# Kernel tuning notes

Hardware: AMD Instinct MI355X
Metric: run time of the kernel (lower is better)

The kernel has to match this reference:

```python
import jax, jax.numpy as jnp
import numpy as np

B, A, C = 16, 16384, 81
TOP_K = 50
CONF_THRESH = 0.5
IOU_THRESH = 0.5
VAR0, VAR1 = 0.1, 0.2          # cfg['variance']
IMG_HW = 1.0                   # cfg['min_dim']/img_size = 320/320
MIN_SIZE = 0.0
NEG = -jnp.inf


def setup_inputs() -> dict:
    key = jax.random.key(0)
    k1, k2, k3 = jax.random.split(key, 3)
    conf_preds = jax.random.uniform(k1, (B, A, C), dtype=jnp.float32)
    loc_delta = jax.random.normal(k2, (B, A, 4), dtype=jnp.float32)
    anchors = jax.random.uniform(k3, (A, 4), dtype=jnp.float32)  # cxcywh priors in [0,1)
    return {"conf_preds": conf_preds, "loc_delta": loc_delta, "anchors": anchors}


def _decode_clip(loc, anchors):
    # SSD decode: cxcy = prior_cxcy + loc_xy*v0*prior_wh ; wh = prior_wh*exp(loc_wh*v1)
    cxcy = anchors[..., :2] + loc[..., :2] * VAR0 * anchors[..., 2:]
    wh = anchors[..., 2:] * jnp.exp(loc[..., 2:] * VAR1)
    x1y1 = cxcy - wh * 0.5
    x2y2 = x1y1 + wh
    boxes = jnp.concatenate([x1y1, x2y2], axis=-1)  # [..., 4] xyxy
    return jnp.clip(boxes, 0.0, IMG_HW)            # clip_boxes_to_image((1,1))


def _nms_single(boxes, s):
    # boxes: [A,4] xyxy, s: [A] scores with invalid entries already at -inf.
    # Greedy NMS, fixed TOP_K iterations (torchvision semantics: suppress iou > thresh).
    areas = (boxes[:, 2] - boxes[:, 0]) * (boxes[:, 3] - boxes[:, 1])

    def step(s, _):
        i = jnp.argmax(s)
        take = s[i] > NEG
        b = boxes[i]
        xx1 = jnp.maximum(b[0], boxes[:, 0])
        yy1 = jnp.maximum(b[1], boxes[:, 1])
        xx2 = jnp.minimum(b[2], boxes[:, 2])
        yy2 = jnp.minimum(b[3], boxes[:, 3])
        inter = jnp.maximum(xx2 - xx1, 0.0) * jnp.maximum(yy2 - yy1, 0.0)
        iou = inter / (areas[i] + areas - inter)
        s = jnp.where(take & (iou > IOU_THRESH), NEG, s)
        s = s.at[i].set(NEG)  # guarantee progress
        return s, (i, take)

    _, (idx, take) = jax.lax.scan(step, s, None, length=TOP_K)
    return idx, take  # [TOP_K] int, [TOP_K] bool


def reference(conf_preds, loc_delta, anchors):
    boxes = _decode_clip(loc_delta, anchors)                # [B,A,4]
    conf = jnp.transpose(conf_preds, (0, 2, 1))             # [B,C,A]
    # remove_small_boxes(min_size=0) as a mask (all-true here, kept for fidelity)
    w = boxes[..., 2] - boxes[..., 0]
    h = boxes[..., 3] - boxes[..., 1]
    valid = (w >= MIN_SIZE) & (h >= MIN_SIZE)               # [B,A]
    masked = jnp.where((conf > CONF_THRESH) & valid[:, None, :], conf, NEG)  # [B,C,A]

    sg = jax.lax.stop_gradient
    nms_c = jax.vmap(_nms_single, in_axes=(None, 0))        # over classes
    nms_bc = jax.vmap(nms_c, in_axes=(0, 0))                # over batch
    idx, take = nms_bc(sg(boxes), sg(masked))               # [B,C,K]

    scores_sel = jnp.take_along_axis(conf, idx, axis=2)     # [B,C,K]
    b_idx = jnp.arange(boxes.shape[0])[:, None, None]
    boxes_sel = boxes[b_idx, idx]                           # [B,C,K,4]
    preds = jnp.concatenate([
        jnp.where(take, scores_sel, 0.0)[..., None],
        jnp.where(take[..., None], boxes_sel, 0.0),
    ], axis=-1)                                             # [B,C,K,5]
    return preds
```

## Files before the change

### kernel.cpp

```cpp
#include <hip/hip_runtime.h>
#include <math.h>

#define NB 16
#define NA 16384
#define NC 81
#define TOPK 50
#define NBK 255
#define TRC 1024
#define NEGF (-__builtin_inff())
#define SUPC 0.5000000298023223876953125

typedef unsigned long long ull;

#define WS_CONFT_OFF  ((size_t)4194304)
#define WS_FULL  (WS_CONFT_OFF + (size_t)NB * NC * NA)

__device__ __forceinline__ bool iou_gt_half(float inter, float den) {
    return fmaf(den, -0.5f, inter) > den * 0x1p-25f;
}

__device__ __forceinline__ unsigned enc8(float v) {
    unsigned e = 0xFFu;
    if (v > 0.5f) {
        unsigned d = 255u - ((__float_as_uint(v) >> 15) & 0xFFu);
        e = (d > 254u) ? 254u : d;
    }
    return e;
}

__device__ __forceinline__ void decode_body(int i, const float* __restrict__ loc,
                                            const float* __restrict__ anc,
                                            float* __restrict__ boxes) {
#pragma clang fp contract(off)
    int a = i & (NA - 1);
    float4 an = ((const float4*)anc)[a];
    float4 ld = ((const float4*)loc)[i];
    float cx = an.x + (ld.x * 0.1f) * an.z;
    float cy = an.y + (ld.y * 0.1f) * an.w;
    float w = an.z * (float)exp((double)(ld.z * 0.2f));
    float h = an.w * (float)exp((double)(ld.w * 0.2f));
    float x1 = cx - w * 0.5f;
    float y1 = cy - h * 0.5f;
    float x2 = x1 + w;
    float y2 = y1 + h;
    x1 = fminf(fmaxf(x1, 0.f), 1.f);
    y1 = fminf(fmaxf(y1, 0.f), 1.f);
    x2 = fminf(fmaxf(x2, 0.f), 1.f);
    y2 = fminf(fmaxf(y2, 0.f), 1.f);
    ((float4*)boxes)[i] = make_float4(x1, y1, x2, y2);
}

__global__ __launch_bounds__(256) void decode_k(const float* __restrict__ loc,
                                                const float* __restrict__ anc,
                                                float* __restrict__ boxes) {
    int i = blockIdx.x * 256 + threadIdx.x;
    if (i < NB * NA) decode_body(i, loc, anc, boxes);
}

#define TSLAB 256
__global__ __launch_bounds__(256) void prep_k(const float* __restrict__ conf,
                                              const float* __restrict__ loc,
                                              const float* __restrict__ anc,
                                              float* __restrict__ boxes,
                                              unsigned char* __restrict__ confT) {
    __shared__ unsigned char code[TSLAB * NC];
    const int t = threadIdx.x;
    const int b = blockIdx.y, slab = blockIdx.x;
    decode_body(b * NA + slab * TSLAB + t, loc, anc, boxes);
    const float4* src = (const float4*)(conf + ((size_t)b * NA + (size_t)slab * TSLAB) * NC);
    for (int i = t; i < (TSLAB * NC) / 4; i += 256) {
        float4 v = src[i];
        unsigned wrd = enc8(v.x) | (enc8(v.y) << 8) | (enc8(v.z) << 16) | (enc8(v.w) << 24);
        *(unsigned*)&code[4 * i] = wrd;
    }
    __syncthreads();
    const int lane = t & 63, wv = t >> 6;
    for (int c = wv; c < NC; c += 4) {
        unsigned v = 0u;
#pragma unroll
        for (int j = 0; j < 4; ++j)
            v |= (unsigned)code[(4 * lane + j) * NC + c] << (8 * j);
        *(unsigned*)(confT + ((size_t)b * NC + c) * NA + (size_t)slab * TSLAB + 4 * lane) = v;
    }
}

#define HIST16(Q)                                                          \
    do {                                                                   \
        unsigned wrds_[4] = {(Q).x, (Q).y, (Q).z, (Q).w};                  \
        _Pragma("unroll")                                                  \
        for (int m_ = 0; m_ < 4; ++m_) {                                   \
            _Pragma("unroll")                                              \
            for (int k_ = 0; k_ < 4; ++k_) {                               \
                unsigned bk_ = (wrds_[m_] >> (8 * k_)) & 0xFFu;            \
                if (bk_ != 0xFFu) atomicAdd(&s_hist[wv][bk_], 1u);         \
            }                                                              \
        }                                                                  \
    } while (0)

#define SCAT16(Q, BA)                                                      \
    do {                                                                   \
        unsigned wrds_[4] = {(Q).x, (Q).y, (Q).z, (Q).w};                  \
        _Pragma("unroll")                                                  \
        for (int m_ = 0; m_ < 4; ++m_) {                                   \
            _Pragma("unroll")                                              \
            for (int k_ = 0; k_ < 4; ++k_) {                               \
                int bk_ = (int)((wrds_[m_] >> (8 * k_)) & 0xFFu);          \
                if (bk_ >= trLo && bk_ < trHi)                             \
                    s_ix[atomicAdd(&s_cur[bk_], 1u)] =                     \
                        (unsigned short)((BA) + 4 * m_ + k_);              \
            }                                                              \
        }                                                                  \
    } while (0)

__global__ __launch_bounds__(256, 8) void nmsB12_k(const unsigned char* __restrict__ confT,
                                                   const float* __restrict__ conf,
                                                   const float* __restrict__ boxes,
                                                   float* __restrict__ out) {
#pragma clang fp contract(off)
    const int blk = blockIdx.x;
    const int b = blk / NC, c = blk - b * NC;
    const int t = threadIdx.x;
    const int lane = t & 63, wv = t >> 6;

    __shared__ unsigned short s_ix[TRC];
    __shared__ unsigned s_off[NBK + 1];
    __shared__ unsigned s_hist[4][NBK + 2];
    __shared__ unsigned s_cur[NBK];
    __shared__ unsigned s_wsum[4];
    __shared__ float4 s_abox[TOPK];
    __shared__ float s_aarea[TOPK];
    __shared__ float4 s_cbox[256];
    __shared__ unsigned long long s_kill[4];
    __shared__ int s_ctrl[16];

    const uint4* row16 = (const uint4*)(confT + ((size_t)b * NC + c) * NA);
    const float* cp = conf + ((size_t)b * NA) * NC + c;
    const float4* bb = (const float4*)boxes + (size_t)b * NA;
    float* orow = out + ((size_t)b * NC + c) * (TOPK * 5);

    for (int i = t; i < 4 * (NBK + 2); i += 256) ((unsigned*)s_hist)[i] = 0u;
    if (t == 0) { s_ctrl[0] = 0; s_ctrl[8] = 0; s_ctrl[12] = 0; }
    __syncthreads();

#pragma unroll
    for (int r = 0; r < 4; ++r) {
        uint4 q = row16[t + 256 * r];
        HIST16(q);
    }
    __syncthreads();

    unsigned cnt = 0u;
    if (t < NBK) {
        cnt = s_hist[0][t] + s_hist[1][t] + s_hist[2][t] + s_hist[3][t];
        atomicMax(&s_ctrl[8], (int)cnt);
    }
    unsigned v = cnt;
#pragma unroll
    for (int off = 1; off < 64; off <<= 1) {
        unsigned o = __shfl_up(v, off);
        if (lane >= off) v += o;
    }
    if (lane == 63) s_wsum[wv] = v;
    __syncthreads();
    unsigned basep = 0u;
    for (int w2 = 0; w2 < wv; ++w2) basep += s_wsum[w2];
    v += basep;
    if (t < NBK) s_off[t + 1] = v;
    if (t == 0) s_off[0] = 0u;
    __syncthreads();

    if (s_ctrl[8] <= TRC) {
        while (true) {
            if (t == 0) {
                int lo = s_ctrl[12];
                int hi = lo;
                while (hi < NBK && s_off[hi + 1] - s_off[lo] <= (unsigned)TRC) hi++;
                s_ctrl[13] = hi;
            }
            __syncthreads();
            const int trLo = s_ctrl[12], trHi = s_ctrl[13];
            const unsigned tbase = s_off[trLo], tend = s_off[trHi];
            if (tbase == tend) break;
            for (int i = trLo + t; i < trHi; i += 256) s_cur[i] = s_off[i] - tbase;
            __syncthreads();
#pragma unroll
            for (int r = 0; r < 4; ++r) {
                uint4 q = row16[t + 256 * r];
                SCAT16(q, 16 * (t + 256 * r));
            }
            if (t == 0) s_ctrl[7] = trLo;
            __syncthreads();

            while (true) {
                if (t == 0) {
                    int bp = s_ctrl[7];
                    int mode;
                    if (bp >= trHi || s_off[bp] >= tend) {
                        mode = 2;
                    } else {
                        unsigned pos = s_off[bp] - tbase;
                        int bpl = bp;
                        unsigned q = pos;
                        for (int w = 0; w < 4; ++w) {
                            s_ctrl[2 + w] = (int)q;
                            while (bpl < trHi && (s_off[bpl + 1] - tbase - q) <= 64u) bpl++;
                            q = (bpl < trHi) ? s_off[bpl] - tbase : tend - tbase;
                        }
                        s_ctrl[6] = (int)q;
                        s_ctrl[7] = bpl;
                        mode = 0;
                        if (q == pos) {
                            mode = 1;
                            s_ctrl[9] = (int)pos;
                            s_ctrl[10] = (int)(s_off[bp + 1] - tbase);
                            s_ctrl[7] = bp + 1;
                        }
                    }
                    s_ctrl[11] = mode;
                }
                __syncthreads();
                const int mode = s_ctrl[11];
                if (mode == 2) break;
                const int nacc0 = s_ctrl[0];

                if (mode == 0) {
                    const unsigned q0 = (unsigned)s_ctrl[2 + wv];
                    const unsigned q1 = (unsigned)s_ctrl[3 + wv];
                    const int mw = (int)(q1 - q0);
                    const bool valid = lane < mw;
                    int ii = (int)q0 + lane; if (ii > TRC - 1) ii = TRC - 1;
                    int a = valid ? (int)s_ix[ii] : 0;
                    float4 bxv = bb[a];
                    if (!valid) bxv = make_float4(0.f, 0.f, 0.f, 0.f);
                    s_cbox[wv * 64 + lane] = bxv;
                    float mar = (bxv.z - bxv.x) * (bxv.w - bxv.y);
                    bool kill = !valid;
                    for (int j = 0; j < nacc0; ++j) {
                        float4 ab = s_abox[j];
                        float aa = s_aarea[j];
                        float xx1 = fmaxf(ab.x, bxv.x), yy1 = fmaxf(ab.y, bxv.y);
                        float xx2 = fminf(ab.z, bxv.z), yy2 = fminf(ab.w, bxv.w);
                        float iw = fmaxf(xx2 - xx1, 0.f), ih = fmaxf(yy2 - yy1, 0.f);
                        float inter = iw * ih;
                        float den = (aa + mar) - inter;
                        if (iou_gt_half(inter, den)) kill = true;
                        if ((j & 7) == 7 && __ballot(kill) == ~0ull) break;
                    }
                    unsigned long long km = __ballot(kill);
                    if (lane == 0) s_kill[wv] = km;
                    __syncthreads();

                    if (wv == 0) {
                        int na = nacc0;
                        for (int cc = 0; cc < 4 && na < TOPK; ++cc) {
                            const unsigned e0 = (unsigned)s_ctrl[2 + cc];
                            const unsigned e1 = (unsigned)s_ctrl[3 + cc];
                            const int mc = (int)(e1 - e0);
                            if (mc <= 0) continue;
                            unsigned long long alive = ~s_kill[cc];
                            if (mc < 64) alive &= (1ull << mc) - 1ull;
                            int jj = (int)e0 + lane; if (jj > TRC - 1) jj = TRC - 1;
                            int aj = (lane < mc) ? (int)s_ix[jj] : 0;
                            float myscore = cp[(size_t)aj * NC];
                            float4 mybx = s_cbox[cc * 64 + lane];
                            float mar2 = (mybx.z - mybx.x) * (mybx.w - mybx.y);
                            for (int j = nacc0; j < na && alive; ++j) {
                                float4 ab = s_abox[j];
                                float aa = s_aarea[j];
                                float xx1 = fmaxf(ab.x, mybx.x), yy1 = fmaxf(ab.y, mybx.y);
                                float xx2 = fminf(ab.z, mybx.z), yy2 = fminf(ab.w, mybx.w);
                                float iw = fmaxf(xx2 - xx1, 0.f), ih = fmaxf(yy2 - yy1, 0.f);
                                float inter = iw * ih;
                                float den = (aa + mar2) - inter;
                                bool sup = iou_gt_half(inter, den);
                                alive &= ~__ballot(sup);
                            }
                            unsigned long long mykey =
                                ((unsigned long long)__float_as_uint(myscore) << 32) |
                                (unsigned)(16383 - aj);
                            while (alive && na < TOPK) {
                                unsigned long long kk = ((alive >> lane) & 1ull) ? mykey : 0ull;
                                int src = lane;
                                for (int off = 32; off; off >>= 1) {
                                    unsigned long long ok = __shfl_xor(kk, off);
                                    int osrc = __shfl_xor(src, off);
                                    if (ok > kk) { kk = ok; src = osrc; }
                                }
                                float4 wb = s_cbox[cc * 64 + src];
                                float wscore = __shfl(myscore, src);
                                float war = (wb.z - wb.x) * (wb.w - wb.y);
                                if (lane == 0) {
                                    orow[na * 5 + 0] = wscore;
                                    orow[na * 5 + 1] = wb.x; orow[na * 5 + 2] = wb.y;
                                    orow[na * 5 + 3] = wb.z; orow[na * 5 + 4] = wb.w;
                                    s_abox[na] = wb;
                                    s_aarea[na] = war;
                                }
                                na++;
                                alive &= ~(1ull << src);
                                if (alive) {
                                    float xx1 = fmaxf(wb.x, mybx.x), yy1 = fmaxf(wb.y, mybx.y);
                                    float xx2 = fminf(wb.z, mybx.z), yy2 = fminf(wb.w, mybx.w);
                                    float iw = fmaxf(xx2 - xx1, 0.f), ih = fmaxf(yy2 - yy1, 0.f);
                                    float inter = iw * ih;
                                    float den = (war + mar2) - inter;
                                    bool sup = iou_gt_half(inter, den);
                                    alive &= ~__ballot(sup);
                                }
                            }
                        }
                        if (lane == 0) s_ctrl[0] = na;
                    }
                    __syncthreads();
                } else {
                    const int e0 = s_ctrl[9], e1 = s_ctrl[10];
                    if (wv == 0) {
                        int na = s_ctrl[0];
                        while (na < TOPK) {
                            unsigned long long bk = 0ull; int bpos = 0;
                            for (int i = e0 + lane; i < e1; i += 64) {
                                int av = (int)s_ix[i];
                                if (av != 0xFFFF) {
                                    float vv = cp[(size_t)av * NC];
                                    unsigned long long k =
                                        ((unsigned long long)__float_as_uint(vv) << 32) |
                                        (unsigned)(16383 - av);
                                    if (k > bk) { bk = k; bpos = i; }
                                }
                            }
                            for (int off = 32; off; off >>= 1) {
                                unsigned long long ok = __shfl_xor(bk, off);
                                int op = __shfl_xor(bpos, off);
                                if (ok > bk) { bk = ok; bpos = op; }
                            }
                            if (bk == 0ull) break;
                            int a = (int)s_ix[bpos];
                            float wscore = __uint_as_float((unsigned)(bk >> 32));
                            if (lane == 0) s_ix[bpos] = 0xFFFFu;
                            float4 wb = bb[a];
                            float war = (wb.z - wb.x) * (wb.w - wb.y);
                            bool sup = false;
                            if (lane < na) {
                                float4 ab = s_abox[lane];
                                float aa = s_aarea[lane];
                                float xx1 = fmaxf(ab.x, wb.x), yy1 = fmaxf(ab.y, wb.y);
                                float xx2 = fminf(ab.z, wb.z), yy2 = fminf(ab.w, wb.w);
                                float iw = fmaxf(xx2 - xx1, 0.f), ih = fmaxf(yy2 - yy1, 0.f);
                                float inter = iw * ih;
                                float den = (aa + war) - inter;
                                sup = iou_gt_half(inter, den);
                            }
                            if (__ballot(sup) == 0ull) {
                                if (lane == 0) {
                                    orow[na * 5 + 0] = wscore;
                                    orow[na * 5 + 1] = wb.x; orow[na * 5 + 2] = wb.y;
                                    orow[na * 5 + 3] = wb.z; orow[na * 5 + 4] = wb.w;
                                    s_abox[na] = wb;
                                    s_aarea[na] = war;
                                }
                                na++;
                            }
                        }
                        if (lane == 0) s_ctrl[0] = na;
                    }
                    __syncthreads();
                }
                if (s_ctrl[0] >= TOPK) break;
            }
            if (s_ctrl[0] >= TOPK || trHi >= NBK) break;
            if (t == 0) s_ctrl[12] = trHi;
            __syncthreads();
        }
    } else {
        float hi = 1.0f, delta = 0.02f;
        while (true) {
            if (s_ctrl[0] >= TOPK || hi <= 0.5f) break;
            float lo = fmaxf(hi - delta, 0.5f);
            if (t == 0) s_ctrl[1] = 0;
            __syncthreads();
            for (int a = t; a < NA; a += 256) {
                float vv = cp[(size_t)a * NC];
                if (vv > lo && vv <= hi) {
                    int p = atomicAdd(&s_ctrl[1], 1);
                    if (p < TRC) s_ix[p] = (unsigned short)a;
                }
            }
            __syncthreads();
            int m = s_ctrl[1];
            if (m > TRC) { delta *= 0.5f; continue; }
            if (wv == 0) {
                int na = s_ctrl[0];
                while (na < TOPK) {
                    unsigned long long bk = 0ull; int bpos = 0;
                    for (int i = lane; i < m; i += 64) {
                        int av = (int)s_ix[i];
                        if (av != 0xFFFF) {
                            float vv = cp[(size_t)av * NC];
                            unsigned long long k =
                                ((unsigned long long)__float_as_uint(vv) << 32) |
                                (unsigned)(16383 - av);
                            if (k > bk) { bk = k; bpos = i; }
                        }
                    }
                    for (int off = 32; off; off >>= 1) {
                        unsigned long long ok = __shfl_xor(bk, off);
                        int op = __shfl_xor(bpos, off);
                        if (ok > bk) { bk = ok; bpos = op; }
                    }
                    if (bk == 0ull) break;
                    int a = (int)s_ix[bpos];
                    float wscore = __uint_as_float((unsigned)(bk >> 32));
                    if (lane == 0) s_ix[bpos] = 0xFFFFu;
                    float4 wb = bb[a];
                    float war = (wb.z - wb.x) * (wb.w - wb.y);
                    bool sup = false;
                    if (lane < na) {
                        float4 ab = s_abox[lane];
                        float aa = s_aarea[lane];
                        float xx1 = fmaxf(ab.x, wb.x), yy1 = fmaxf(ab.y, wb.y);
                        float xx2 = fminf(ab.z, wb.z), yy2 = fminf(ab.w, wb.w);
                        float iw = fmaxf(xx2 - xx1, 0.f), ih = fmaxf(yy2 - yy1, 0.f);
                        float inter = iw * ih;
                        float den = (aa + war) - inter;
                        sup = iou_gt_half(inter, den);
                    }
                    if (__ballot(sup) == 0ull) {
                        if (lane == 0) {
                            orow[na * 5 + 0] = wscore;
                            orow[na * 5 + 1] = wb.x; orow[na * 5 + 2] = wb.y;
                            orow[na * 5 + 3] = wb.z; orow[na * 5 + 4] = wb.w;
                            s_abox[na] = wb;
                            s_aarea[na] = war;
                        }
                        na++;
                    }
                }
                if (lane == 0) s_ctrl[0] = na;
            }
            __syncthreads();
            hi = lo;
        }
    }

    __syncthreads();
    const int naF = s_ctrl[0];
    for (int z = naF * 5 + t; z < TOPK * 5; z += 256) orow[z] = 0.f;
}

#define OTHREADS 1024
#define OCAP 10240
#define OJMAX 10

__global__ __launch_bounds__(OTHREADS) void nms_old_k(const float* __restrict__ conf,
                                                      const float* __restrict__ boxes,
                                                      float* __restrict__ out) {
#pragma clang fp contract(off)
    const int blk = blockIdx.x;
    const int b = blk / NC, c = blk - b * NC;
    const int t = threadIdx.x;
    const int lane = t & 63, wid = t >> 6;
    __shared__ float s_val[OCAP];
    __shared__ unsigned short s_idx[OCAP];
    __shared__ float s_ps[2][16];
    __shared__ int s_pa[2][16];
    __shared__ int s_n;
    if (t == 0) s_n = 0;
    __syncthreads();
    const float* cp = conf + ((size_t)b * NA) * NC + c;
    float v[NA / OTHREADS];
#pragma unroll
    for (int r = 0; r < NA / OTHREADS; ++r)
        v[r] = cp[(size_t)(r * OTHREADS + t) * NC];
#pragma unroll
    for (int r = 0; r < NA / OTHREADS; ++r) {
        int a = r * OTHREADS + t;
        bool alive = v[r] > 0.5f;
        unsigned long long m = __ballot(alive);
        int cnt = __popcll(m);
        int base = 0;
        if (lane == 0 && cnt) base = atomicAdd(&s_n, cnt);
        base = __shfl(base, 0);
        if (alive) {
            int p = base + __popcll(m & ((1ull << lane) - 1));
            if (p < OCAP) { s_val[p] = v[r]; s_idx[p] = (unsigned short)a; }
        }
    }
    __syncthreads();
    int n = s_n; if (n > OCAP) n = OCAP;
    const int jn = (n + OTHREADS - 1) / OTHREADS;
    const float4* bb = (const float4*)boxes + (size_t)b * NA;
    float sc[OJMAX]; float4 bx[OJMAX]; int ia[OJMAX];
#pragma unroll
    for (int j = 0; j < OJMAX; ++j) {
        sc[j] = NEGF; ia[j] = 0x7fffffff; bx[j] = make_float4(0.f, 0.f, 0.f, 0.f);
        int p = j * OTHREADS + t;
        if (p < n) { sc[j] = s_val[p]; ia[j] = (int)s_idx[p]; bx[j] = bb[ia[j]]; }
    }
    float* orow = out + (size_t)blk * (TOPK * 5);
    int k = 0;
    for (; k < TOPK; ++k) {
        float ms = NEGF; int ma = 0x7fffffff;
#pragma unroll
        for (int j = 0; j < OJMAX; ++j) {
            if (j < jn) {
                bool better = (sc[j] > ms) || (sc[j] == ms && ia[j] < ma);
                ms = better ? sc[j] : ms;
                ma = better ? ia[j] : ma;
            }
        }
#pragma unroll
        for (int off = 32; off; off >>= 1) {
            float os = __shfl_xor(ms, off);
            int oa = __shfl_xor(ma, off);
            if (os > ms || (os == ms && oa < ma)) { ms = os; ma = oa; }
        }
        int pb = k & 1;
        if (lane == 0) { s_ps[pb][wid] = ms; s_pa[pb][wid] = ma; }
        __syncthreads();
        float wsv = NEGF; int wa = 0x7fffffff;
#pragma unroll
        for (int w = 0; w < 16; ++w) {
            float os = s_ps[pb][w]; int oa = s_pa[pb][w];
            if (os > wsv || (os == wsv && oa < wa)) { wsv = os; wa = oa; }
        }
        if (!(wsv > NEGF)) break;
        float4 wb = bb[wa];
        float warea = (wb.z - wb.x) * (wb.w - wb.y);
        if (t == 0) {
            orow[k * 5 + 0] = wsv;
            orow[k * 5 + 1] = wb.x; orow[k * 5 + 2] = wb.y;
            orow[k * 5 + 3] = wb.z; orow[k * 5 + 4] = wb.w;
        }
#pragma unroll
        for (int j = 0; j < OJMAX; ++j) {
            if (j < jn) {
                float xx1 = fmaxf(wb.x, bx[j].x);
                float yy1 = fmaxf(wb.y, bx[j].y);
                float xx2 = fminf(wb.z, bx[j].z);
                float yy2 = fminf(wb.w, bx[j].w);
                float iw = fmaxf(xx2 - xx1, 0.f);
                float ih = fmaxf(yy2 - yy1, 0.f);
                float inter = iw * ih;
                float aj = (bx[j].z - bx[j].x) * (bx[j].w - bx[j].y);
                float denom = (warea + aj) - inter;
                bool supp = ((double)inter > (double)denom * SUPC) || (ia[j] == wa);
                if (supp) sc[j] = NEGF;
            }
        }
    }
    for (int z = k * 5 + t; z < TOPK * 5; z += OTHREADS) orow[z] = 0.f;
}

extern "C" void kernel_launch(void* const* d_in, const int* in_sizes, int n_in,
                              void* d_out, int out_size, void* d_ws, size_t ws_size,
                              hipStream_t stream) {
    const float* conf = (const float*)d_in[0];
    const float* loc  = (const float*)d_in[1];
    const float* anc  = (const float*)d_in[2];
    float* boxes = (float*)d_ws;

    if (ws_size >= WS_FULL) {
        unsigned char* confT = (unsigned char*)((char*)d_ws + WS_CONFT_OFF);
        dim3 tg(NA / TSLAB, NB);
        prep_k<<<tg, 256, 0, stream>>>(conf, loc, anc, boxes, confT);
        nmsB12_k<<<NB * NC, 256, 0, stream>>>(confT, conf, boxes, (float*)d_out);
    } else {
        decode_k<<<(NB * NA + 255) / 256, 256, 0, stream>>>(loc, anc, boxes);
        nms_old_k<<<NB * NC, OTHREADS, 0, stream>>>(conf, boxes, (float*)d_out);
    }
}
```

Before: 194.0 us.

## Rewrite per-class NMS kernel as a single-wavefront block without barriers

Replaces the 256-thread per-(batch,class) NMS kernel with a 64-thread single-wavefront version. Control state moves from shared memory to registers, the per-wave histograms collapse into one shared count array, and the 4-wave candidate chunking with a wave-0 serial merge becomes one 64-candidate chunk per step. It also prefetches the next chunk's boxes while the current chunk is processed. The goal is to remove block-wide barriers and thread-0 serial control, at the cost of less parallelism for the histogram/scatter pass and the IoU tests against accepted boxes, plus more shared-atomic contention on a single histogram.

```diff
diff --git a/kernel.cpp b/kernel.cpp
--- a/kernel.cpp
+++ b/kernel.cpp
@@ -84,7 +84,7 @@
     }
 }
 
-#define HIST16(Q)                                                          \
+#define HIST16W(Q)                                                         \
     do {                                                                   \
         unsigned wrds_[4] = {(Q).x, (Q).y, (Q).z, (Q).w};                  \
         _Pragma("unroll")                                                  \
@@ -92,12 +92,12 @@
             _Pragma("unroll")                                              \
             for (int k_ = 0; k_ < 4; ++k_) {                               \
                 unsigned bk_ = (wrds_[m_] >> (8 * k_)) & 0xFFu;            \
-                if (bk_ != 0xFFu) atomicAdd(&s_hist[wv][bk_], 1u);         \
+                if (bk_ != 0xFFu) atomicAdd(&s_cnt[bk_], 1u);              \
             }                                                              \
         }                                                                  \
     } while (0)
 
-#define SCAT16(Q, BA)                                                      \
+#define SCAT16W(Q, BA)                                                     \
     do {                                                                   \
         unsigned wrds_[4] = {(Q).x, (Q).y, (Q).z, (Q).w};                  \
         _Pragma("unroll")                                                  \
@@ -112,130 +112,121 @@
         }                                                                  \
     } while (0)
 
-__global__ __launch_bounds__(256, 8) void nmsB12_k(const unsigned char* __restrict__ confT,
-                                                   const float* __restrict__ conf,
-                                                   const float* __restrict__ boxes,
-                                                   float* __restrict__ out) {
+__global__ __launch_bounds__(64, 4) void nmsW_k(const unsigned char* __restrict__ confT,
+                                                const float* __restrict__ conf,
+                                                const float* __restrict__ boxes,
+                                                float* __restrict__ out) {
 #pragma clang fp contract(off)
     const int blk = blockIdx.x;
     const int b = blk / NC, c = blk - b * NC;
-    const int t = threadIdx.x;
-    const int lane = t & 63, wv = t >> 6;
+    const int lane = threadIdx.x;
 
     __shared__ unsigned short s_ix[TRC];
     __shared__ unsigned s_off[NBK + 1];
-    __shared__ unsigned s_hist[4][NBK + 2];
+    __shared__ unsigned s_cnt[NBK + 1];
     __shared__ unsigned s_cur[NBK];
-    __shared__ unsigned s_wsum[4];
     __shared__ float4 s_abox[TOPK];
     __shared__ float s_aarea[TOPK];
-    __shared__ float4 s_cbox[256];
-    __shared__ unsigned long long s_kill[4];
-    __shared__ int s_ctrl[16];
+    __shared__ int s_m;
 
     const uint4* row16 = (const uint4*)(confT + ((size_t)b * NC + c) * NA);
     const float* cp = conf + ((size_t)b * NA) * NC + c;
     const float4* bb = (const float4*)boxes + (size_t)b * NA;
     float* orow = out + ((size_t)b * NC + c) * (TOPK * 5);
 
-    for (int i = t; i < 4 * (NBK + 2); i += 256) ((unsigned*)s_hist)[i] = 0u;
-    if (t == 0) { s_ctrl[0] = 0; s_ctrl[8] = 0; s_ctrl[12] = 0; }
+#pragma unroll
+    for (int k = 0; k < 4; ++k) s_cnt[4 * lane + k] = 0u;
     __syncthreads();
 
-#pragma unroll
-    for (int r = 0; r < 4; ++r) {
-        uint4 q = row16[t + 256 * r];
-        HIST16(q);
+    for (int r = 0; r < 16; ++r) {
+        uint4 q = row16[lane + 64 * r];
+        HIST16W(q);
     }
     __syncthreads();
 
-    unsigned cnt = 0u;
-    if (t < NBK) {
-        cnt = s_hist[0][t] + s_hist[1][t] + s_hist[2][t] + s_hist[3][t];
-        atomicMax(&s_ctrl[8], (int)cnt);
-    }
-    unsigned v = cnt;
+    unsigned c4[4]; unsigned tot = 0u, maxb = 0u;
+#pragma unroll
+    for (int k = 0; k < 4; ++k) {
+        int idx = 4 * lane + k;
+        c4[k] = (idx < NBK) ? s_cnt[idx] : 0u;
+        tot += c4[k];
+        maxb = (c4[k] > maxb) ? c4[k] : maxb;
+    }
+#pragma unroll
+    for (int off = 32; off; off >>= 1) {
+        unsigned o = __shfl_xor(maxb, off);
+        maxb = (o > maxb) ? o : maxb;
+    }
+    unsigned incl = tot;
 #pragma unroll
     for (int off = 1; off < 64; off <<= 1) {
-        unsigned o = __shfl_up(v, off);
-        if (lane >= off) v += o;
-    }
-    if (lane == 63) s_wsum[wv] = v;
+        unsigned o = __shfl_up(incl, off);
+        if (lane >= off) incl += o;
+    }
+    unsigned e = incl - tot;
+#pragma unroll
+    for (int k = 0; k < 4; ++k) {
+        int idx = 4 * lane + k;
+        if (idx < NBK) s_off[idx] = e;
+        e += c4[k];
+    }
+    if (lane == 63) s_off[NBK] = e;
     __syncthreads();
-    unsigned basep = 0u;
-    for (int w2 = 0; w2 < wv; ++w2) basep += s_wsum[w2];
-    v += basep;
-    if (t < NBK) s_off[t + 1] = v;
-    if (t == 0) s_off[0] = 0u;
-    __syncthreads();
-
-    if (s_ctrl[8] <= TRC) {
+
+    int nacc = 0;
+
+    if (maxb <= (unsigned)TRC) {
+        int trLo = 0;
         while (true) {
-            if (t == 0) {
-                int lo = s_ctrl[12];
-                int hi = lo;
-                while (hi < NBK && s_off[hi + 1] - s_off[lo] <= (unsigned)TRC) hi++;
-                s_ctrl[13] = hi;
+            int trHi = trLo;
+            while (trHi < NBK && s_off[trHi + 1] - s_off[trLo] <= (unsigned)TRC) trHi++;
+            const unsigned tbase = s_off[trLo], tend = s_off[trHi];
+            if (tbase == tend) break;
+            const int tlen = (int)(tend - tbase);
+            for (int i = trLo + lane; i < trHi; i += 64) s_cur[i] = s_off[i] - tbase;
+            __syncthreads();
+            for (int r = 0; r < 16; ++r) {
+                uint4 q = row16[lane + 64 * r];
+                SCAT16W(q, 16 * (lane + 64 * r));
             }
             __syncthreads();
-            const int trLo = s_ctrl[12], trHi = s_ctrl[13];
-            const unsigned tbase = s_off[trLo], tend = s_off[trHi];
-            if (tbase == tend) break;
-            for (int i = trLo + t; i < trHi; i += 256) s_cur[i] = s_off[i] - tbase;
-            __syncthreads();
-#pragma unroll
-            for (int r = 0; r < 4; ++r) {
-                uint4 q = row16[t + 256 * r];
-                SCAT16(q, 16 * (t + 256 * r));
-            }
-            if (t == 0) s_ctrl[7] = trLo;
-            __syncthreads();
-
-            while (true) {
-                if (t == 0) {
-                    int bp = s_ctrl[7];
-                    int mode;
-                    if (bp >= trHi || s_off[bp] >= tend) {
-                        mode = 2;
-                    } else {
-                        unsigned pos = s_off[bp] - tbase;
-                        int bpl = bp;
-                        unsigned q = pos;
-                        for (int w = 0; w < 4; ++w) {
-                            s_ctrl[2 + w] = (int)q;
-                            while (bpl < trHi && (s_off[bpl + 1] - tbase - q) <= 64u) bpl++;
-                            q = (bpl < trHi) ? s_off[bpl] - tbase : tend - tbase;
-                        }
-                        s_ctrl[6] = (int)q;
-                        s_ctrl[7] = bpl;
-                        mode = 0;
-                        if (q == pos) {
-                            mode = 1;
-                            s_ctrl[9] = (int)pos;
-                            s_ctrl[10] = (int)(s_off[bp + 1] - tbase);
-                            s_ctrl[7] = bp + 1;
-                        }
+
+            int bptr = trLo;
+            int pf_pos = -1;
+            float4 pf_box = make_float4(0.f, 0.f, 0.f, 0.f);
+
+            while (nacc < TOPK) {
+                if (bptr >= trHi || (int)(s_off[bptr] - tbase) >= tlen) break;
+                const int e0 = (int)(s_off[bptr] - tbase);
+                int bpl = bptr;
+                while (bpl < trHi && (int)(s_off[bpl + 1] - tbase) - e0 <= 64) bpl++;
+                int e1 = (bpl < trHi) ? (int)(s_off[bpl] - tbase) : tlen;
+                int mode = 0;
+                if (e1 == e0) {
+                    mode = 1;
+                    e1 = (int)(s_off[bptr + 1] - tbase);
+                    bptr = bptr + 1;
+                } else {
+                    bptr = bpl;
+                }
+
+                if (mode == 0) {
+                    const int mc = e1 - e0;
+                    const bool valid = lane < mc;
+                    int ii = e0 + lane; if (ii > TRC - 1) ii = TRC - 1;
+                    int a = valid ? (int)s_ix[ii] : 0;
+                    float4 bxv = (pf_pos == e0) ? pf_box : bb[a];
+                    float myscore = valid ? cp[(size_t)a * NC] : 0.f;
+                    if (!valid) bxv = make_float4(0.f, 0.f, 0.f, 0.f);
+                    float mar = (bxv.z - bxv.x) * (bxv.w - bxv.y);
+                    {
+                        int pi = e1 + lane; if (pi > TRC - 1) pi = TRC - 1;
+                        int pa = (e1 + lane < tlen) ? (int)s_ix[pi] : 0;
+                        pf_box = bb[pa];
+                        pf_pos = e1;
                     }
-                    s_ctrl[11] = mode;
-                }
-                __syncthreads();
-                const int mode = s_ctrl[11];
-                if (mode == 2) break;
-                const int nacc0 = s_ctrl[0];
-
-                if (mode == 0) {
-                    const unsigned q0 = (unsigned)s_ctrl[2 + wv];
-                    const unsigned q1 = (unsigned)s_ctrl[3 + wv];
-                    const int mw = (int)(q1 - q0);
-                    const bool valid = lane < mw;
-                    int ii = (int)q0 + lane; if (ii > TRC - 1) ii = TRC - 1;
-                    int a = valid ? (int)s_ix[ii] : 0;
-                    float4 bxv = bb[a];
-                    if (!valid) bxv = make_float4(0.f, 0.f, 0.f, 0.f);
-                    s_cbox[wv * 64 + lane] = bxv;
-                    float mar = (bxv.z - bxv.x) * (bxv.w - bxv.y);
                     bool kill = !valid;
-                    for (int j = 0; j < nacc0; ++j) {
+                    for (int j = 0; j < nacc; ++j) {
                         float4 ab = s_abox[j];
                         float aa = s_aarea[j];
                         float xx1 = fmaxf(ab.x, bxv.x), yy1 = fmaxf(ab.y, bxv.y);
@@ -244,207 +235,169 @@
                         float inter = iw * ih;
                         float den = (aa + mar) - inter;
                         if (iou_gt_half(inter, den)) kill = true;
-                        if ((j & 7) == 7 && __ballot(kill) == ~0ull) break;
                     }
-                    unsigned long long km = __ballot(kill);
-                    if (lane == 0) s_kill[wv] = km;
-                    __syncthreads();
-
-                    if (wv == 0) {
-                        int na = nacc0;
-                        for (int cc = 0; cc < 4 && na < TOPK; ++cc) {
-                            const unsigned e0 = (unsigned)s_ctrl[2 + cc];
-                            const unsigned e1 = (unsigned)s_ctrl[3 + cc];
-                            const int mc = (int)(e1 - e0);
-                            if (mc <= 0) continue;
-                            unsigned long long alive = ~s_kill[cc];
-                            if (mc < 64) alive &= (1ull << mc) - 1ull;
-                            int jj = (int)e0 + lane; if (jj > TRC - 1) jj = TRC - 1;
-                            int aj = (lane < mc) ? (int)s_ix[jj] : 0;
-                            float myscore = cp[(size_t)aj * NC];
-                            float4 mybx = s_cbox[cc * 64 + lane];
-                            float mar2 = (mybx.z - mybx.x) * (mybx.w - mybx.y);
-                            for (int j = nacc0; j < na && alive; ++j) {
-                                float4 ab = s_abox[j];
-                                float aa = s_aarea[j];
-                                float xx1 = fmaxf(ab.x, mybx.x), yy1 = fmaxf(ab.y, mybx.y);
-                                float xx2 = fminf(ab.z, mybx.z), yy2 = fminf(ab.w, mybx.w);
-                                float iw = fmaxf(xx2 - xx1, 0.f), ih = fmaxf(yy2 - yy1, 0.f);
-                                float inter = iw * ih;
-                                float den = (aa + mar2) - inter;
-                                bool sup = iou_gt_half(inter, den);
-                                alive &= ~__ballot(sup);
-                            }
-                            unsigned long long mykey =
-                                ((unsigned long long)__float_as_uint(myscore) << 32) |
-                                (unsigned)(16383 - aj);
-                            while (alive && na < TOPK) {
-                                unsigned long long kk = ((alive >> lane) & 1ull) ? mykey : 0ull;
-                                int src = lane;
-                                for (int off = 32; off; off >>= 1) {
-                                    unsigned long long ok = __shfl_xor(kk, off);
-                                    int osrc = __shfl_xor(src, off);
-                                    if (ok > kk) { kk = ok; src = osrc; }
-                                }
-                                float4 wb = s_cbox[cc * 64 + src];
-                                float wscore = __shfl(myscore, src);
-                                float war = (wb.z - wb.x) * (wb.w - wb.y);
-                                if (lane == 0) {
-                                    orow[na * 5 + 0] = wscore;
-                                    orow[na * 5 + 1] = wb.x; orow[na * 5 + 2] = wb.y;
-                                    orow[na * 5 + 3] = wb.z; orow[na * 5 + 4] = wb.w;
-                                    s_abox[na] = wb;
-                                    s_aarea[na] = war;
-                                }
-                                na++;
-                                alive &= ~(1ull << src);
-                                if (alive) {
-                                    float xx1 = fmaxf(wb.x, mybx.x), yy1 = fmaxf(wb.y, mybx.y);
-                                    float xx2 = fminf(wb.z, mybx.z), yy2 = fminf(wb.w, mybx.w);
-                                    float iw = fmaxf(xx2 - xx1, 0.f), ih = fmaxf(yy2 - yy1, 0.f);
-                                    float inter = iw * ih;
-                                    float den = (war + mar2) - inter;
-                                    bool sup = iou_gt_half(inter, den);
-                                    alive &= ~__ballot(sup);
-                                }
-                            }
-                        }
-                        if (lane == 0) s_ctrl[0] = na;
+                    unsigned long long alive = ~__ballot(kill);
+                    if (mc < 64) alive &= (1ull << mc) - 1ull;
+                    unsigned long long mykey =
+                        ((unsigned long long)__float_as_uint(myscore) << 32) |
+                        (unsigned)(16383 - a);
+                    while (alive && nacc < TOPK) {
+                        unsigned long long kk = ((alive >> lane) & 1ull) ? mykey : 0ull;
+                        int src = lane;
+#pragma unroll
+                        for (int off = 32; off; off >>= 1) {
+                            unsigned long long ok = __shfl_xor(kk, off);
+                            int osrc = __shfl_xor(src, off);
+                            if (ok > kk) { kk = ok; src = osrc; }
+                        }
+                        float wx = __shfl(bxv.x, src), wy = __shfl(bxv.y, src);
+                        float wz = __shfl(bxv.z, src), ww = __shfl(bxv.w, src);
+                        float wscore = __shfl(myscore, src);
+                        float war = (wz - wx) * (ww - wy);
+                        if (lane == 0) {
+                            orow[nacc * 5 + 0] = wscore;
+                            orow[nacc * 5 + 1] = wx; orow[nacc * 5 + 2] = wy;
+                            orow[nacc * 5 + 3] = wz; orow[nacc * 5 + 4] = ww;
+                            s_abox[nacc] = make_float4(wx, wy, wz, ww);
+                            s_aarea[nacc] = war;
+                        }
+                        nacc++;
+                        alive &= ~(1ull << src);
+                        if (alive) {
+                            float xx1 = fmaxf(wx, bxv.x), yy1 = fmaxf(wy, bxv.y);
+                            float xx2 = fminf(wz, bxv.z), yy2 = fminf(ww, bxv.w);
+                            float iw = fmaxf(xx2 - xx1, 0.f), ih = fmaxf(yy2 - yy1, 0.f);
+                            float inter = iw * ih;
+                            float den = (war + mar) - inter;
+                            bool sup = iou_gt_half(inter, den);
+                            alive &= ~__ballot(sup);
+                        }
                     }
                     __syncthreads();
                 } else {
-                    const int e0 = s_ctrl[9], e1 = s_ctrl[10];
-                    if (wv == 0) {
-                        int na = s_ctrl[0];
-                        while (na < TOPK) {
-                            unsigned long long bk = 0ull; int bpos = 0;
-                            for (int i = e0 + lane; i < e1; i += 64) {
-                                int av = (int)s_ix[i];
-                                if (av != 0xFFFF) {
-                                    float vv = cp[(size_t)av * NC];
-                                    unsigned long long k =
-                                        ((unsigned long long)__float_as_uint(vv) << 32) |
-                                        (unsigned)(16383 - av);
-                                    if (k > bk) { bk = k; bpos = i; }
-                                }
+                    pf_pos = -1;
+                    while (nacc < TOPK) {
+                        unsigned long long bk = 0ull; int bpos = 0;
+                        for (int i = e0 + lane; i < e1; i += 64) {
+                            int av = (int)s_ix[i];
+                            if (av != 0xFFFF) {
+                                float vv = cp[(size_t)av * NC];
+                                unsigned long long k =
+                                    ((unsigned long long)__float_as_uint(vv) << 32) |
+                                    (unsigned)(16383 - av);
+                                if (k > bk) { bk = k; bpos = i; }
                             }
-                            for (int off = 32; off; off >>= 1) {
-                                unsigned long long ok = __shfl_xor(bk, off);
-                                int op = __shfl_xor(bpos, off);
-                                if (ok > bk) { bk = ok; bpos = op; }
+                        }
+#pragma unroll
+                        for (int off = 32; off; off >>= 1) {
+                            unsigned long long ok = __shfl_xor(bk, off);
+                            int op = __shfl_xor(bpos, off);
+                            if (ok > bk) { bk = ok; bpos = op; }
+                        }
+                        if (bk == 0ull) break;
+                        int a = (int)s_ix[bpos];
+                        float wscore = __uint_as_float((unsigned)(bk >> 32));
+                        if (lane == 0) s_ix[bpos] = 0xFFFFu;
+                        float4 wb = bb[a];
+                        float war = (wb.z - wb.x) * (wb.w - wb.y);
+                        bool sup = false;
+                        if (lane < nacc) {
+                            float4 ab = s_abox[lane];
+                            float aa = s_aarea[lane];
+                            float xx1 = fmaxf(ab.x, wb.x), yy1 = fmaxf(ab.y, wb.y);
+                            float xx2 = fminf(ab.z, wb.z), yy2 = fminf(ab.w, wb.w);
+                            float iw = fmaxf(xx2 - xx1, 0.f), ih = fmaxf(yy2 - yy1, 0.f);
+                            float inter = iw * ih;
+                            float den = (aa + war) - inter;
+                            sup = iou_gt_half(inter, den);
+                        }
+                        if (__ballot(sup) == 0ull) {
+                            if (lane == 0) {
+                                orow[nacc * 5 + 0] = wscore;
+                                orow[nacc * 5 + 1] = wb.x; orow[nacc * 5 + 2] = wb.y;
+                                orow[nacc * 5 + 3] = wb.z; orow[nacc * 5 + 4] = wb.w;
+                                s_abox[nacc] = wb;
+                                s_aarea[nacc] = war;
                             }
-                            if (bk == 0ull) break;
-                            int a = (int)s_ix[bpos];
-                            float wscore = __uint_as_float((unsigned)(bk >> 32));
-                            if (lane == 0) s_ix[bpos] = 0xFFFFu;
-                            float4 wb = bb[a];
-                            float war = (wb.z - wb.x) * (wb.w - wb.y);
-                            bool sup = false;
-                            if (lane < na) {
-                                float4 ab = s_abox[lane];
-                                float aa = s_aarea[lane];
-                                float xx1 = fmaxf(ab.x, wb.x), yy1 = fmaxf(ab.y, wb.y);
-                                float xx2 = fminf(ab.z, wb.z), yy2 = fminf(ab.w, wb.w);
-                                float iw = fmaxf(xx2 - xx1, 0.f), ih = fmaxf(yy2 - yy1, 0.f);
-                                float inter = iw * ih;
-                                float den = (aa + war) - inter;
-                                sup = iou_gt_half(inter, den);
-                            }
-                            if (__ballot(sup) == 0ull) {
-                                if (lane == 0) {
-                                    orow[na * 5 + 0] = wscore;
-                                    orow[na * 5 + 1] = wb.x; orow[na * 5 + 2] = wb.y;
-                                    orow[na * 5 + 3] = wb.z; orow[na * 5 + 4] = wb.w;
-                                    s_abox[na] = wb;
-                                    s_aarea[na] = war;
-                                }
-                                na++;
-                            }
-                        }
-                        if (lane == 0) s_ctrl[0] = na;
+                            nacc++;
+                        }
                     }
                     __syncthreads();
                 }
-                if (s_ctrl[0] >= TOPK) break;
             }
-            if (s_ctrl[0] >= TOPK || trHi >= NBK) break;
-            if (t == 0) s_ctrl[12] = trHi;
+            if (nacc >= TOPK || trHi >= NBK) break;
+            trLo = trHi;
             __syncthreads();
         }
     } else {
         float hi = 1.0f, delta = 0.02f;
         while (true) {
-            if (s_ctrl[0] >= TOPK || hi <= 0.5f) break;
+            if (nacc >= TOPK || hi <= 0.5f) break;
             float lo = fmaxf(hi - delta, 0.5f);
-            if (t == 0) s_ctrl[1] = 0;
+            if (lane == 0) s_m = 0;
             __syncthreads();
-            for (int a = t; a < NA; a += 256) {
+            for (int a = lane; a < NA; a += 64) {
                 float vv = cp[(size_t)a * NC];
                 if (vv > lo && vv <= hi) {
-                    int p = atomicAdd(&s_ctrl[1], 1);
+                    int p = atomicAdd(&s_m, 1);
                     if (p < TRC) s_ix[p] = (unsigned short)a;
                 }
             }
             __syncthreads();
-            int m = s_ctrl[1];
+            int m = s_m;
             if (m > TRC) { delta *= 0.5f; continue; }
-            if (wv == 0) {
-                int na = s_ctrl[0];
-                while (na < TOPK) {
-                    unsigned long long bk = 0ull; int bpos = 0;
-                    for (int i = lane; i < m; i += 64) {
-                        int av = (int)s_ix[i];
-                        if (av != 0xFFFF) {
-                            float vv = cp[(size_t)av * NC];
-                            unsigned long long k =
-                                ((unsigned long long)__float_as_uint(vv) << 32) |
-                                (unsigned)(16383 - av);
-                            if (k > bk) { bk = k; bpos = i; }
-                        }
+            while (nacc < TOPK) {
+                unsigned long long bk = 0ull; int bpos = 0;
+                for (int i = lane; i < m; i += 64) {
+                    int av = (int)s_ix[i];
+                    if (av != 0xFFFF) {
+                        float vv = cp[(size_t)av * NC];
+                        unsigned long long k =
+                            ((unsigned long long)__float_as_uint(vv) << 32) |
+                            (unsigned)(16383 - av);
+                        if (k > bk) { bk = k; bpos = i; }
                     }
-                    for (int off = 32; off; off >>= 1) {
-                        unsigned long long ok = __shfl_xor(bk, off);
-                        int op = __shfl_xor(bpos, off);
-                        if (ok > bk) { bk = ok; bpos = op; }
+                }
+#pragma unroll
+                for (int off = 32; off; off >>= 1) {
+                    unsigned long long ok = __shfl_xor(bk, off);
+                    int op = __shfl_xor(bpos, off);
+                    if (ok > bk) { bk = ok; bpos = op; }
+                }
+                if (bk == 0ull) break;
+                int a = (int)s_ix[bpos];
+                float wscore = __uint_as_float((unsigned)(bk >> 32));
+                if (lane == 0) s_ix[bpos] = 0xFFFFu;
+                float4 wb = bb[a];
+                float war = (wb.z - wb.x) * (wb.w - wb.y);
+                bool sup = false;
+                if (lane < nacc) {
+                    float4 ab = s_abox[lane];
+                    float aa = s_aarea[lane];
+                    float xx1 = fmaxf(ab.x, wb.x), yy1 = fmaxf(ab.y, wb.y);
+                    float xx2 = fminf(ab.z, wb.z), yy2 = fminf(ab.w, wb.w);
+                    float iw = fmaxf(xx2 - xx1, 0.f), ih = fmaxf(yy2 - yy1, 0.f);
+                    float inter = iw * ih;
+                    float den = (aa + war) - inter;
+                    sup = iou_gt_half(inter, den);
+                }
+                if (__ballot(sup) == 0ull) {
+                    if (lane == 0) {
+                        orow[nacc * 5 + 0] = wscore;
+                        orow[nacc * 5 + 1] = wb.x; orow[nacc * 5 + 2] = wb.y;
+                        orow[nacc * 5 + 3] = wb.z; orow[nacc * 5 + 4] = wb.w;
+                        s_abox[nacc] = wb;
+                        s_aarea[nacc] = war;
                     }
-                    if (bk == 0ull) break;
-                    int a = (int)s_ix[bpos];
-                    float wscore = __uint_as_float((unsigned)(bk >> 32));
-                    if (lane == 0) s_ix[bpos] = 0xFFFFu;
-                    float4 wb = bb[a];
-                    float war = (wb.z - wb.x) * (wb.w - wb.y);
-                    bool sup = false;
-                    if (lane < na) {
-                        float4 ab = s_abox[lane];
-                        float aa = s_aarea[lane];
-                        float xx1 = fmaxf(ab.x, wb.x), yy1 = fmaxf(ab.y, wb.y);
-                        float xx2 = fminf(ab.z, wb.z), yy2 = fminf(ab.w, wb.w);
-                        float iw = fmaxf(xx2 - xx1, 0.f), ih = fmaxf(yy2 - yy1, 0.f);
-                        float inter = iw * ih;
-                        float den = (aa + war) - inter;
-                        sup = iou_gt_half(inter, den);
-                    }
-                    if (__ballot(sup) == 0ull) {
-                        if (lane == 0) {
-                            orow[na * 5 + 0] = wscore;
-                            orow[na * 5 + 1] = wb.x; orow[na * 5 + 2] = wb.y;
-                            orow[na * 5 + 3] = wb.z; orow[na * 5 + 4] = wb.w;
-                            s_abox[na] = wb;
-                            s_aarea[na] = war;
-                        }
-                        na++;
-                    }
-                }
-                if (lane == 0) s_ctrl[0] = na;
+                    nacc++;
+                }
             }
             __syncthreads();
             hi = lo;
         }
     }
 
-    __syncthreads();
-    const int naF = s_ctrl[0];
-    for (int z = naF * 5 + t; z < TOPK * 5; z += 256) orow[z] = 0.f;
+    for (int z = nacc * 5 + lane; z < TOPK * 5; z += 64) orow[z] = 0.f;
 }
 
 #define OTHREADS 1024
@@ -563,7 +516,7 @@
         unsigned char* confT = (unsigned char*)((char*)d_ws + WS_CONFT_OFF);
         dim3 tg(NA / TSLAB, NB);
         prep_k<<<tg, 256, 0, stream>>>(conf, loc, anc, boxes, confT);
-        nmsB12_k<<<NB * NC, 256, 0, stream>>>(confT, conf, boxes, (float*)d_out);
+        nmsW_k<<<NB * NC, 64, 0, stream>>>(confT, conf, boxes, (float*)d_out);
     } else {
         decode_k<<<(NB * NA + 255) / 256, 256, 0, stream>>>(loc, anc, boxes);
         nms_old_k<<<NB * NC, OTHREADS, 0, stream>>>(conf, boxes, (float*)d_out);
```

Measured after the change: 204.0 us. +5.1%, slower.
